# Performance work log

Hardware: AMD Instinct MI355X
Metric: run time of the kernel (lower is better)

Reference implementation:

```python
import jax, jax.numpy as jnp
import numpy as np

N_HEADS = 16

def setup_inputs() -> dict:
    key = jax.random.key(0)
    k1, k2, k3 = jax.random.split(key, 3)
    d = 1024
    x = jax.random.normal(k1, (4, 2048, d), dtype=jnp.float32)
    w_qkv = jax.random.normal(k2, (d, 3 * d), dtype=jnp.float32) * (1.0 / np.sqrt(d))
    w_proj = jax.random.normal(k3, (d, d), dtype=jnp.float32) * (1.0 / np.sqrt(d))
    return {"x": x, "w_qkv": w_qkv, "w_proj": w_proj}

def reference(x, w_qkv, w_proj):
    b, s, c = x.shape
    h = N_HEADS
    hd = c // h
    qkv = x @ w_qkv  # [b, s, 3c]
    q, k, v = jnp.split(qkv, 3, axis=-1)
    # [b, h, s, hd]
    q = q.reshape(b, s, h, hd).transpose(0, 2, 1, 3)
    k = k.reshape(b, s, h, hd).transpose(0, 2, 1, 3)
    v = v.reshape(b, s, h, hd).transpose(0, 2, 1, 3)
    scores = jnp.einsum('bhqd,bhkd->bhqk', q, k) / jnp.sqrt(jnp.float32(hd))
    causal = jnp.tril(jnp.ones((s, s), dtype=bool))
    scores = jnp.where(causal[None, None], scores, jnp.float32(-jnp.inf))
    attn = jax.nn.softmax(scores, axis=-1)
    out = jnp.einsum('bhqk,bhkd->bhqd', attn, v)
    out = out.transpose(0, 2, 1, 3).reshape(b, s, c)
    return out @ w_proj
```

## Files before the change

kernel.cpp:

```cpp
#include <hip/hip_runtime.h>
#include <hip/hip_bf16.h>

typedef unsigned short u16;
typedef __attribute__((ext_vector_type(8))) short short8;
typedef __attribute__((ext_vector_type(4))) float f32x4;
typedef __attribute__((ext_vector_type(16))) float f32x16;

__device__ inline u16 f2bf(float f) {
  unsigned u = __float_as_uint(f);
  u += 0x7fffu + ((u >> 16) & 1u);
  return (u16)(u >> 16);
}

__global__ __launch_bounds__(256) void cast_kernel(const float* __restrict__ in,
                                                   u16* __restrict__ out, int n4) {
  int i = blockIdx.x * 256 + threadIdx.x;
  if (i >= n4) return;
  float4 v = ((const float4*)in)[i];
  ushort4 o;
  o.x = f2bf(v.x); o.y = f2bf(v.y); o.z = f2bf(v.z); o.w = f2bf(v.w);
  ((ushort4*)out)[i] = o;
}

__global__ __launch_bounds__(256) void tcast_kernel(const float* __restrict__ in,
                                                    u16* __restrict__ out, int K, int N) {
  __shared__ float tile[32][33];
  int bx = blockIdx.x * 32;
  int by = blockIdx.y * 32;
  int tx = threadIdx.x & 31, ty = threadIdx.x >> 5;
#pragma unroll
  for (int i = 0; i < 4; i++) {
    int r = ty + i * 8;
    tile[r][tx] = in[(size_t)(by + r) * N + bx + tx];
  }
  __syncthreads();
#pragma unroll
  for (int i = 0; i < 4; i++) {
    int r = ty + i * 8;
    out[(size_t)(bx + r) * K + by + tx] = f2bf(tile[tx][r]);
  }
}

__global__ __launch_bounds__(256) void pack_kv(const u16* __restrict__ kbuf,
                                               const u16* __restrict__ vbuf,
                                               u16* __restrict__ kpack,
                                               u16* __restrict__ vpack) {
  __shared__ __align__(16) u16 ktile[64 * 72];
  __shared__ __align__(16) u16 vtile[64 * 72];
  int t = threadIdx.x;
  int kt = blockIdx.x, h = blockIdx.y, b = blockIdx.z;
  int bh = b * 16 + h;
  size_t rb = (size_t)(b * 2048 + kt * 64);
#pragma unroll
  for (int i = 0; i < 2; i++) {
    int idx = i * 256 + t; int r = idx >> 3, c8 = (idx & 7) * 8;
    *(uint4*)&ktile[r * 72 + c8] = *(const uint4*)(kbuf + (rb + r) * 1024 + h * 64 + c8);
    *(uint4*)&vtile[r * 72 + c8] = *(const uint4*)(vbuf + (rb + r) * 1024 + h * 64 + c8);
  }
  __syncthreads();
  u16* kd = kpack + ((size_t)bh * 32 + kt) * 4096;
  u16* vd = vpack + ((size_t)bh * 32 + kt) * 4096;
#pragma unroll
  for (int i = 0; i < 2; i++) {
    int idx = i * 256 + t;
    int j = idx >> 6, lane = idx & 63, l31 = lane & 31, hi5 = lane >> 5;
    *(uint4*)(kd + j * 512 + lane * 8) =
        *(const uint4*)&ktile[((j >> 2) * 32 + l31) * 72 + (j & 3) * 16 + hi5 * 8];
    union { u16 s[8]; uint4 u; } pv;
#pragma unroll
    for (int e = 0; e < 8; e++)
      pv.s[e] = vtile[((j & 3) * 16 + hi5 * 8 + e) * 72 + (j >> 2) * 32 + l31];
    *(uint4*)(vd + j * 512 + lane * 8) = pv.u;
  }
}

__device__ inline void cstore(float* p, float v) { *p = v; }
__device__ inline void cstore(u16* p, float v) { *p = f2bf(v); }

#define GEMM_BODY(KSTR)                                                                       \
  __shared__ __align__(16) u16 As[128 * 32];                                                  \
  __shared__ __align__(16) u16 Bs[128 * 32];                                                  \
  int t = threadIdx.x;                                                                        \
  int wave = t >> 6, lane = t & 63, l15 = lane & 15, quad = lane >> 4;                        \
  int bn = blockIdx.x * 128, bm = blockIdx.y * 128;                                           \
  int wm = (wave >> 1) * 64, wn = (wave & 1) * 64;                                            \
  f32x4 acc[4][4];                                                                            \
  for (int i = 0; i < 4; i++)                                                                 \
    for (int j = 0; j < 4; j++) acc[i][j] = (f32x4)0.0f;                                      \
  int srow = wave * 16 + (lane >> 2);                                                         \
  int scol = (lane & 3) * 8;                                                                  \
  const u16* ga0 = A + (size_t)(bm + srow) * KSTR + scol;                                     \
  const u16* ga1 = A + (size_t)(bm + 64 + srow) * KSTR + scol;                                \
  const u16* gb0 = Bt + (size_t)(bn + srow) * KSTR + scol;                                    \
  const u16* gb1 = Bt + (size_t)(bn + 64 + srow) * KSTR + scol;                               \
  u16* lA0 = As + wave * 512;                                                                 \
  u16* lA1 = As + 2048 + wave * 512;                                                          \
  u16* lB0 = Bs + wave * 512;                                                                 \
  u16* lB1 = Bs + 2048 + wave * 512;                                                          \
  for (int k0 = 0; k0 < KSTR; k0 += 32) {                                                     \
    __syncthreads();                                                                          \
    __builtin_amdgcn_global_load_lds((const __attribute__((address_space(1))) unsigned*)(ga0 + k0), \
                                     (__attribute__((address_space(3))) unsigned*)lA0, 16, 0, 0);   \
    __builtin_amdgcn_global_load_lds((const __attribute__((address_space(1))) unsigned*)(ga1 + k0), \
                                     (__attribute__((address_space(3))) unsigned*)lA1, 16, 0, 0);   \
    __builtin_amdgcn_global_load_lds((const __attribute__((address_space(1))) unsigned*)(gb0 + k0), \
                                     (__attribute__((address_space(3))) unsigned*)lB0, 16, 0, 0);   \
    __builtin_amdgcn_global_load_lds((const __attribute__((address_space(1))) unsigned*)(gb1 + k0), \
                                     (__attribute__((address_space(3))) unsigned*)lB1, 16, 0, 0);   \
    __syncthreads();                                                                          \
    short8 a[4], b[4];                                                                        \
    for (int mt = 0; mt < 4; mt++)                                                            \
      a[mt] = *(const short8*)(&As[(wm + mt * 16 + l15) * 32 + quad * 8]);                    \
    for (int nt = 0; nt < 4; nt++)                                                            \
      b[nt] = *(const short8*)(&Bs[(wn + nt * 16 + l15) * 32 + quad * 8]);                    \
    for (int mt = 0; mt < 4; mt++)                                                            \
      for (int nt = 0; nt < 4; nt++)                                                          \
        acc[mt][nt] = __builtin_amdgcn_mfma_f32_16x16x32_bf16(a[mt], b[nt], acc[mt][nt], 0, 0, 0); \
  }

__global__ __launch_bounds__(256) void gemm_qkv(const u16* __restrict__ A,
                                                const u16* __restrict__ Bt,
                                                u16* __restrict__ qb,
                                                u16* __restrict__ kb,
                                                u16* __restrict__ vb) {
  GEMM_BODY(1024)
  u16* dst = (bn < 1024) ? qb : (bn < 2048) ? kb : vb;
  int bnl = bn & 1023;
#pragma unroll
  for (int mt = 0; mt < 4; mt++)
#pragma unroll
    for (int nt = 0; nt < 4; nt++)
#pragma unroll
      for (int r = 0; r < 4; r++) {
        int row = bm + wm + mt * 16 + quad * 4 + r;
        int col = bnl + wn + nt * 16 + l15;
        dst[(size_t)row * 1024 + col] = f2bf(acc[mt][nt][r]);
      }
}

__global__ __launch_bounds__(256) void gemm_proj(const u16* __restrict__ A,
                                                 const u16* __restrict__ Bt,
                                                 float* __restrict__ Co) {
  GEMM_BODY(1024)
#pragma unroll
  for (int mt = 0; mt < 4; mt++)
#pragma unroll
    for (int nt = 0; nt < 4; nt++)
#pragma unroll
      for (int r = 0; r < 4; r++) {
        int row = bm + wm + mt * 16 + quad * 4 + r;
        int col = bn + wn + nt * 16 + l15;
        Co[(size_t)row * 1024 + col] = acc[mt][nt][r];
      }
}

__global__ __launch_bounds__(256, 2) void attn_kernel(const u16* __restrict__ qbuf,
                                                      const u16* __restrict__ kpack,
                                                      const u16* __restrict__ vpack,
                                                      u16* __restrict__ ctx) {
  int t = threadIdx.x;
  int wave = t >> 6, lane = t & 63, l31 = lane & 31, hi = lane >> 5;
  int lid = (int)blockIdx.x + 16 * (int)blockIdx.y + 256 * (int)blockIdx.z;
  int xcd = lid & 7, slot = lid >> 3;
  int bh = xcd + 8 * (slot & 7);
  int i = slot >> 3;
  int b = bh >> 4, h = bh & 15;
  int ww = (wave + i) & 3;
  int strip = (ww == 0) ? i : (ww == 1) ? 31 - i : (ww == 2) ? 32 + i : 63 - i;
  int rowbase = b * 2048;
  int q0 = strip * 32;
  int q_lane = q0 + l31;
  const float SCL = 0.18033688011112f;

  const u16* qp = qbuf + (size_t)(rowbase + q_lane) * 1024 + h * 64 + hi * 8;
  short8 qf[4];
#pragma unroll
  for (int ks = 0; ks < 4; ks++) qf[ks] = *(const short8*)(qp + ks * 16);

  const u16* kp = kpack + (size_t)bh * (32 * 4096) + lane * 8;
  const u16* vp = vpack + (size_t)bh * (32 * 4096) + lane * 8;

  float m_run = -1e30f, l_run = 0.0f;
  f32x16 o[2];
  o[0] = (f32x16)0.0f; o[1] = (f32x16)0.0f;
  int hi4 = hi * 4;
  int ktmax = (q0 + 31) >> 6;

  for (int kt = 0; kt <= ktmax; kt++) {
    const u16* kb = kp + kt * 4096;
    const u16* vb = vp + kt * 4096;

    short8 ka[8], vv[8];
#pragma unroll
    for (int j = 0; j < 8; j++) {
      ka[j] = *(const short8*)(kb + j * 512);
      vv[j] = *(const short8*)(vb + j * 512);
    }

    f32x16 st0 = (f32x16)0.0f, st1 = (f32x16)0.0f;
#pragma unroll
    for (int ks = 0; ks < 4; ks++) {
      st0 = __builtin_amdgcn_mfma_f32_32x32x16_bf16(ka[ks], qf[ks], st0, 0, 0, 0);
      st1 = __builtin_amdgcn_mfma_f32_32x32x16_bf16(ka[4 + ks], qf[ks], st1, 0, 0, 0);
    }

    float sc[2][16];
    if (kt == ktmax) {
#pragma unroll
      for (int r = 0; r < 16; r++) {
        int key = kt * 64 + (r & 3) + 8 * (r >> 2) + hi4;
        sc[0][r] = (key <= q_lane) ? st0[r] * SCL : -1e30f;
        sc[1][r] = (key + 32 <= q_lane) ? st1[r] * SCL : -1e30f;
      }
    } else {
#pragma unroll
      for (int r = 0; r < 16; r++) { sc[0][r] = st0[r] * SCL; sc[1][r] = st1[r] * SCL; }
    }

    float mo = -1e30f;
#pragma unroll
    for (int r = 0; r < 16; r++) mo = fmaxf(mo, fmaxf(sc[0][r], sc[1][r]));
    mo = fmaxf(mo, __shfl_xor(mo, 32));
    float mnew = fmaxf(m_run, mo);
    float alpha = __builtin_amdgcn_exp2f(m_run - mnew);
    m_run = mnew;
    float rs = 0.0f;
    unsigned pk[2][8];
#pragma unroll
    for (int km = 0; km < 2; km++)
#pragma unroll
      for (int ii = 0; ii < 8; ii++) {
        float p0 = __builtin_amdgcn_exp2f(sc[km][2 * ii] - mnew);
        float p1 = __builtin_amdgcn_exp2f(sc[km][2 * ii + 1] - mnew);
        rs += p0 + p1;
        unsigned lo = (__float_as_uint(p0) + 0x8000u) >> 16;
        unsigned hi_ = (__float_as_uint(p1) + 0x8000u) & 0xffff0000u;
        pk[km][ii] = lo | hi_;
      }
    rs += __shfl_xor(rs, 32);
    l_run = l_run * alpha + rs;
    o[0] = o[0] * alpha;
    o[1] = o[1] * alpha;

    short8 pf[4];
#pragma unroll
    for (int ks2 = 0; ks2 < 4; ks2++) {
      int km = ks2 >> 1, h4 = (ks2 & 1) * 4;
      unsigned A0 = pk[km][h4 + 0], A1 = pk[km][h4 + 1];
      unsigned B0 = pk[km][h4 + 2], B1 = pk[km][h4 + 3];
      unsigned tA0 = (unsigned)__shfl_xor((int)A0, 32);
      unsigned tA1 = (unsigned)__shfl_xor((int)A1, 32);
      unsigned tB0 = (unsigned)__shfl_xor((int)B0, 32);
      unsigned tB1 = (unsigned)__shfl_xor((int)B1, 32);
      union { unsigned u[4]; short8 s; } fr;
      fr.u[0] = hi ? tB0 : A0;
      fr.u[1] = hi ? tB1 : A1;
      fr.u[2] = hi ? B0 : tA0;
      fr.u[3] = hi ? B1 : tA1;
      pf[ks2] = fr.s;
    }

#pragma unroll
    for (int am = 0; am < 2; am++)
#pragma unroll
      for (int ks2 = 0; ks2 < 4; ks2++)
        o[am] = __builtin_amdgcn_mfma_f32_32x32x16_bf16(vv[am * 4 + ks2], pf[ks2], o[am], 0, 0, 0);
  }

  float inv = 1.0f / l_run;
  size_t obase = (size_t)(rowbase + q_lane) * 1024 + h * 64;
#pragma unroll
  for (int am = 0; am < 2; am++)
#pragma unroll
    for (int k = 0; k < 4; k++) {
      ushort4 w;
      w.x = f2bf(o[am][4 * k + 0] * inv);
      w.y = f2bf(o[am][4 * k + 1] * inv);
      w.z = f2bf(o[am][4 * k + 2] * inv);
      w.w = f2bf(o[am][4 * k + 3] * inv);
      *(ushort4*)&ctx[obase + am * 32 + k * 8 + hi4] = w;
    }
}

extern "C" void kernel_launch(void* const* d_in, const int* in_sizes, int n_in,
                              void* d_out, int out_size, void* d_ws, size_t ws_size,
                              hipStream_t stream) {
  const float* x      = (const float*)d_in[0];
  const float* w_qkv  = (const float*)d_in[1];
  const float* w_proj = (const float*)d_in[2];
  float* out = (float*)d_out;

  char* ws = (char*)d_ws;
  const size_t MB = 1024 * 1024;
  u16* qbuf   = (u16*)(ws);
  u16* kbuf   = (u16*)(ws + 16 * MB);
  u16* vbuf   = (u16*)(ws + 32 * MB);
  u16* xb     = (u16*)(ws + 48 * MB);
  u16* kpack  = (u16*)(ws + 48 * MB);
  u16* vpack  = (u16*)(ws + 64 * MB);
  u16* wqkvT  = (u16*)(ws + 80 * MB);
  u16* wprojT = (u16*)(ws + 86 * MB);
  u16* ctx    = kbuf;

  cast_kernel<<<8192, 256, 0, stream>>>(x, xb, 2097152);
  tcast_kernel<<<dim3(96, 32), 256, 0, stream>>>(w_qkv, wqkvT, 1024, 3072);
  tcast_kernel<<<dim3(32, 32), 256, 0, stream>>>(w_proj, wprojT, 1024, 1024);

  gemm_qkv<<<dim3(24, 64), 256, 0, stream>>>(xb, wqkvT, qbuf, kbuf, vbuf);
  pack_kv<<<dim3(32, 16, 4), 256, 0, stream>>>(kbuf, vbuf, kpack, vpack);
  attn_kernel<<<dim3(16, 16, 4), 256, 0, stream>>>(qbuf, kpack, vpack, ctx);
  gemm_proj<<<dim3(8, 64), 256, 0, stream>>>(ctx, wprojT, out);
}
```

Before: 281.6 us.

## Pair causal query strips per wave and fold softmax scale into QKV GEMM

```diff
diff --git a/kernel.cpp b/kernel.cpp
--- a/kernel.cpp
+++ b/kernel.cpp
@@ -73,9 +73,6 @@
     *(uint4*)(vd + j * 512 + lane * 8) = pv.u;
   }
 }
-
-__device__ inline void cstore(float* p, float v) { *p = v; }
-__device__ inline void cstore(u16* p, float v) { *p = f2bf(v); }
 
 #define GEMM_BODY(KSTR)                                                                       \
   __shared__ __align__(16) u16 As[128 * 32];                                                  \
@@ -125,6 +122,7 @@
                                                 u16* __restrict__ vb) {
   GEMM_BODY(1024)
   u16* dst = (bn < 1024) ? qb : (bn < 2048) ? kb : vb;
+  float scl = (bn < 1024) ? 0.18033688011112f : 1.0f;
   int bnl = bn & 1023;
 #pragma unroll
   for (int mt = 0; mt < 4; mt++)
@@ -134,7 +132,7 @@
       for (int r = 0; r < 4; r++) {
         int row = bm + wm + mt * 16 + quad * 4 + r;
         int col = bnl + wn + nt * 16 + l15;
-        dst[(size_t)row * 1024 + col] = f2bf(acc[mt][nt][r]);
+        dst[(size_t)row * 1024 + col] = f2bf(acc[mt][nt][r] * scl);
       }
 }
 
@@ -160,126 +158,126 @@
                                                       u16* __restrict__ ctx) {
   int t = threadIdx.x;
   int wave = t >> 6, lane = t & 63, l31 = lane & 31, hi = lane >> 5;
-  int lid = (int)blockIdx.x + 16 * (int)blockIdx.y + 256 * (int)blockIdx.z;
-  int xcd = lid & 7, slot = lid >> 3;
-  int bh = xcd + 8 * (slot & 7);
-  int i = slot >> 3;
+  int bh = blockIdx.x;
+  int s = (int)blockIdx.y * 4 + wave;
   int b = bh >> 4, h = bh & 15;
-  int ww = (wave + i) & 3;
-  int strip = (ww == 0) ? i : (ww == 1) ? 31 - i : (ww == 2) ? 32 + i : 63 - i;
   int rowbase = b * 2048;
-  int q0 = strip * 32;
-  int q_lane = q0 + l31;
-  const float SCL = 0.18033688011112f;
-
-  const u16* qp = qbuf + (size_t)(rowbase + q_lane) * 1024 + h * 64 + hi * 8;
-  short8 qf[4];
-#pragma unroll
-  for (int ks = 0; ks < 4; ks++) qf[ks] = *(const short8*)(qp + ks * 16);
+  int hi4 = hi * 4;
 
   const u16* kp = kpack + (size_t)bh * (32 * 4096) + lane * 8;
   const u16* vp = vpack + (size_t)bh * (32 * 4096) + lane * 8;
 
-  float m_run = -1e30f, l_run = 0.0f;
-  f32x16 o[2];
-  o[0] = (f32x16)0.0f; o[1] = (f32x16)0.0f;
-  int hi4 = hi * 4;
-  int ktmax = (q0 + 31) >> 6;
-
-  for (int kt = 0; kt <= ktmax; kt++) {
-    const u16* kb = kp + kt * 4096;
-    const u16* vb = vp + kt * 4096;
-
-    short8 ka[8], vv[8];
-#pragma unroll
-    for (int j = 0; j < 8; j++) {
-      ka[j] = *(const short8*)(kb + j * 512);
-      vv[j] = *(const short8*)(vb + j * 512);
+#pragma unroll
+  for (int ph = 0; ph < 2; ph++) {
+    int strip = ph ? 63 - s : s;
+    int q0 = strip * 32;
+    int q_lane = q0 + l31;
+
+    const u16* qp = qbuf + (size_t)(rowbase + q_lane) * 1024 + h * 64 + hi * 8;
+    short8 qf[4];
+#pragma unroll
+    for (int ks = 0; ks < 4; ks++) qf[ks] = *(const short8*)(qp + ks * 16);
+
+    float m_run = -1e30f, l_run = 0.0f;
+    f32x16 o[2];
+    o[0] = (f32x16)0.0f; o[1] = (f32x16)0.0f;
+    int ktmax = (q0 + 31) >> 6;
+
+    for (int kt = 0; kt <= ktmax; kt++) {
+      const u16* kb = kp + kt * 4096;
+      const u16* vb = vp + kt * 4096;
+
+      short8 ka[8], vv[8];
+#pragma unroll
+      for (int j = 0; j < 8; j++) {
+        ka[j] = *(const short8*)(kb + j * 512);
+        vv[j] = *(const short8*)(vb + j * 512);
+      }
+
+      f32x16 st0 = (f32x16)0.0f, st1 = (f32x16)0.0f;
+#pragma unroll
+      for (int ks = 0; ks < 4; ks++) {
+        st0 = __builtin_amdgcn_mfma_f32_32x32x16_bf16(ka[ks], qf[ks], st0, 0, 0, 0);
+        st1 = __builtin_amdgcn_mfma_f32_32x32x16_bf16(ka[4 + ks], qf[ks], st1, 0, 0, 0);
+      }
+
+      float sc[2][16];
+      if (kt == ktmax) {
+#pragma unroll
+        for (int r = 0; r < 16; r++) {
+          int key = kt * 64 + (r & 3) + 8 * (r >> 2) + hi4;
+          sc[0][r] = (key <= q_lane) ? st0[r] : -1e30f;
+          sc[1][r] = (key + 32 <= q_lane) ? st1[r] : -1e30f;
+        }
+      } else {
+#pragma unroll
+        for (int r = 0; r < 16; r++) { sc[0][r] = st0[r]; sc[1][r] = st1[r]; }
+      }
+
+      float mo = -1e30f;
+#pragma unroll
+      for (int r = 0; r < 16; r++) mo = fmaxf(mo, fmaxf(sc[0][r], sc[1][r]));
+      mo = fmaxf(mo, __shfl_xor(mo, 32));
+      float mnew = fmaxf(m_run, mo);
+      float alpha = __builtin_amdgcn_exp2f(m_run - mnew);
+      m_run = mnew;
+      float rs = 0.0f;
+      unsigned pk[2][8];
+#pragma unroll
+      for (int km = 0; km < 2; km++)
+#pragma unroll
+        for (int ii = 0; ii < 8; ii++) {
+          float p0 = __builtin_amdgcn_exp2f(sc[km][2 * ii] - mnew);
+          float p1 = __builtin_amdgcn_exp2f(sc[km][2 * ii + 1] - mnew);
+          rs += p0 + p1;
+          unsigned lo = (__float_as_uint(p0) + 0x8000u) >> 16;
+          unsigned hi_ = (__float_as_uint(p1) + 0x8000u) & 0xffff0000u;
+          pk[km][ii] = lo | hi_;
+        }
+      rs += __shfl_xor(rs, 32);
+      l_run = l_run * alpha + rs;
+      o[0] = o[0] * alpha;
+      o[1] = o[1] * alpha;
+
+      short8 pf[4];
+#pragma unroll
+      for (int ks2 = 0; ks2 < 4; ks2++) {
+        int km = ks2 >> 1, h4 = (ks2 & 1) * 4;
+        unsigned A0 = pk[km][h4 + 0], A1 = pk[km][h4 + 1];
+        unsigned B0 = pk[km][h4 + 2], B1 = pk[km][h4 + 3];
+        unsigned tA0 = (unsigned)__shfl_xor((int)A0, 32);
+        unsigned tA1 = (unsigned)__shfl_xor((int)A1, 32);
+        unsigned tB0 = (unsigned)__shfl_xor((int)B0, 32);
+        unsigned tB1 = (unsigned)__shfl_xor((int)B1, 32);
+        union { unsigned u[4]; short8 sh; } fr;
+        fr.u[0] = hi ? tB0 : A0;
+        fr.u[1] = hi ? tB1 : A1;
+        fr.u[2] = hi ? B0 : tA0;
+        fr.u[3] = hi ? B1 : tA1;
+        pf[ks2] = fr.sh;
+      }
+
+#pragma unroll
+      for (int am = 0; am < 2; am++)
+#pragma unroll
+        for (int ks2 = 0; ks2 < 4; ks2++)
+          o[am] = __builtin_amdgcn_mfma_f32_32x32x16_bf16(vv[am * 4 + ks2], pf[ks2], o[am], 0, 0, 0);
     }
 
-    f32x16 st0 = (f32x16)0.0f, st1 = (f32x16)0.0f;
-#pragma unroll
-    for (int ks = 0; ks < 4; ks++) {
-      st0 = __builtin_amdgcn_mfma_f32_32x32x16_bf16(ka[ks], qf[ks], st0, 0, 0, 0);
-      st1 = __builtin_amdgcn_mfma_f32_32x32x16_bf16(ka[4 + ks], qf[ks], st1, 0, 0, 0);
-    }
-
-    float sc[2][16];
-    if (kt == ktmax) {
-#pragma unroll
-      for (int r = 0; r < 16; r++) {
-        int key = kt * 64 + (r & 3) + 8 * (r >> 2) + hi4;
-        sc[0][r] = (key <= q_lane) ? st0[r] * SCL : -1e30f;
-        sc[1][r] = (key + 32 <= q_lane) ? st1[r] * SCL : -1e30f;
-      }
-    } else {
-#pragma unroll
-      for (int r = 0; r < 16; r++) { sc[0][r] = st0[r] * SCL; sc[1][r] = st1[r] * SCL; }
-    }
-
-    float mo = -1e30f;
-#pragma unroll
-    for (int r = 0; r < 16; r++) mo = fmaxf(mo, fmaxf(sc[0][r], sc[1][r]));
-    mo = fmaxf(mo, __shfl_xor(mo, 32));
-    float mnew = fmaxf(m_run, mo);
-    float alpha = __builtin_amdgcn_exp2f(m_run - mnew);
-    m_run = mnew;
-    float rs = 0.0f;
-    unsigned pk[2][8];
-#pragma unroll
-    for (int km = 0; km < 2; km++)
-#pragma unroll
-      for (int ii = 0; ii < 8; ii++) {
-        float p0 = __builtin_amdgcn_exp2f(sc[km][2 * ii] - mnew);
-        float p1 = __builtin_amdgcn_exp2f(sc[km][2 * ii + 1] - mnew);
-        rs += p0 + p1;
-        unsigned lo = (__float_as_uint(p0) + 0x8000u) >> 16;
-        unsigned hi_ = (__float_as_uint(p1) + 0x8000u) & 0xffff0000u;
-        pk[km][ii] = lo | hi_;
-      }
-    rs += __shfl_xor(rs, 32);
-    l_run = l_run * alpha + rs;
-    o[0] = o[0] * alpha;
-    o[1] = o[1] * alpha;
-
-    short8 pf[4];
-#pragma unroll
-    for (int ks2 = 0; ks2 < 4; ks2++) {
-      int km = ks2 >> 1, h4 = (ks2 & 1) * 4;
-      unsigned A0 = pk[km][h4 + 0], A1 = pk[km][h4 + 1];
-      unsigned B0 = pk[km][h4 + 2], B1 = pk[km][h4 + 3];
-      unsigned tA0 = (unsigned)__shfl_xor((int)A0, 32);
-      unsigned tA1 = (unsigned)__shfl_xor((int)A1, 32);
-      unsigned tB0 = (unsigned)__shfl_xor((int)B0, 32);
-      unsigned tB1 = (unsigned)__shfl_xor((int)B1, 32);
-      union { unsigned u[4]; short8 s; } fr;
-      fr.u[0] = hi ? tB0 : A0;
-      fr.u[1] = hi ? tB1 : A1;
-      fr.u[2] = hi ? B0 : tA0;
-      fr.u[3] = hi ? B1 : tA1;
-      pf[ks2] = fr.s;
-    }
-
+    float inv = 1.0f / l_run;
+    size_t obase = (size_t)(rowbase + q_lane) * 1024 + h * 64;
 #pragma unroll
     for (int am = 0; am < 2; am++)
 #pragma unroll
-      for (int ks2 = 0; ks2 < 4; ks2++)
-        o[am] = __builtin_amdgcn_mfma_f32_32x32x16_bf16(vv[am * 4 + ks2], pf[ks2], o[am], 0, 0, 0);
-  }
-
-  float inv = 1.0f / l_run;
-  size_t obase = (size_t)(rowbase + q_lane) * 1024 + h * 64;
-#pragma unroll
-  for (int am = 0; am < 2; am++)
-#pragma unroll
-    for (int k = 0; k < 4; k++) {
-      ushort4 w;
-      w.x = f2bf(o[am][4 * k + 0] * inv);
-      w.y = f2bf(o[am][4 * k + 1] * inv);
-      w.z = f2bf(o[am][4 * k + 2] * inv);
-      w.w = f2bf(o[am][4 * k + 3] * inv);
-      *(ushort4*)&ctx[obase + am * 32 + k * 8 + hi4] = w;
-    }
+      for (int k = 0; k < 4; k++) {
+        ushort4 w;
+        w.x = f2bf(o[am][4 * k + 0] * inv);
+        w.y = f2bf(o[am][4 * k + 1] * inv);
+        w.z = f2bf(o[am][4 * k + 2] * inv);
+        w.w = f2bf(o[am][4 * k + 3] * inv);
+        *(ushort4*)&ctx[obase + am * 32 + k * 8 + hi4] = w;
+      }
+  }
 }
 
 extern "C" void kernel_launch(void* const* d_in, const int* in_sizes, int n_in,
@@ -308,6 +306,6 @@
 
   gemm_qkv<<<dim3(24, 64), 256, 0, stream>>>(xb, wqkvT, qbuf, kbuf, vbuf);
   pack_kv<<<dim3(32, 16, 4), 256, 0, stream>>>(kbuf, vbuf, kpack, vpack);
-  attn_kernel<<<dim3(16, 16, 4), 256, 0, stream>>>(qbuf, kpack, vpack, ctx);
+  attn_kernel<<<dim3(64, 8), 256, 0, stream>>>(qbuf, kpack, vpack, ctx);
   gemm_proj<<<dim3(8, 64), 256, 0, stream>>>(ctx, wprojT, out);
 }
```

Result: faster. 266.3 us (-5.4%).
